# Optimization experiments

Measured on AMD Instinct MI355X. Metric: run time of the kernel, lower is better.

## Reference

```python
import jax, jax.numpy as jnp
import numpy as np

N_HEAD, D_MODEL, D_HEAD = 16, 1024, 64
LN_EPS = 1e-5
SCALE = 1.0 / (D_HEAD ** 0.5)


def _rel_shift(x):
    # x: [qlen, klen, bsz, n_head]
    q, k, b, n = x.shape
    zero_pad = jnp.zeros((q, 1, b, n), x.dtype)
    x_padded = jnp.concatenate([zero_pad, x], axis=1)        # [q, k+1, b, n]
    x_padded = x_padded.reshape(k + 1, q, b, n)
    return x_padded[1:].reshape(q, k, b, n)


def setup_inputs() -> dict:
    key = jax.random.key(0)
    ks = jax.random.split(key, 8)
    qlen, bsz = 2048, 4
    H = N_HEAD * D_HEAD
    s = 0.02
    return {
        "w": jax.random.normal(ks[0], (qlen, bsz, D_MODEL), jnp.float32),
        "r": jax.random.normal(ks[1], (qlen, D_MODEL), jnp.float32),
        "qkv_w": jax.random.normal(ks[2], (3 * H, D_MODEL), jnp.float32) * s,
        "r_net_w": jax.random.normal(ks[3], (H, D_MODEL), jnp.float32) * s,
        "o_w": jax.random.normal(ks[4], (D_MODEL, H), jnp.float32) * s,
        "r_w_bias": jax.random.normal(ks[5], (N_HEAD, D_HEAD), jnp.float32) * s,
        "r_r_bias": jax.random.normal(ks[6], (N_HEAD, D_HEAD), jnp.float32) * s,
        "ln_g": jnp.ones((D_MODEL,), jnp.float32),
        "ln_b": jnp.zeros((D_MODEL,), jnp.float32),
    }


def _layer_norm(x, g, b):
    mu = jnp.mean(x, axis=-1, keepdims=True)
    var = jnp.var(x, axis=-1, keepdims=True)
    return (x - mu) * jax.lax.rsqrt(var + LN_EPS) * g + b


def reference(w, r, qkv_w, r_net_w, o_w, r_w_bias, r_r_bias, ln_g, ln_b):
    qlen, bsz, _ = w.shape
    rlen = r.shape[0]
    H = N_HEAD * D_HEAD

    w_heads = jnp.einsum('ibm,hm->ibh', w, qkv_w)            # [q,b,3H]
    r_head_k = jnp.einsum('jm,hm->jh', r, r_net_w)           # [r,H]

    w_head_q = w_heads[..., :H].reshape(qlen, bsz, N_HEAD, D_HEAD)
    w_head_k = w_heads[..., H:2 * H].reshape(qlen, bsz, N_HEAD, D_HEAD)
    w_head_v = w_heads[..., 2 * H:].reshape(qlen, bsz, N_HEAD, D_HEAD)
    r_head_k = r_head_k.reshape(rlen, N_HEAD, D_HEAD)

    AC = jnp.einsum('ibnd,jbnd->ijbn', w_head_q + r_w_bias, w_head_k)
    BD = jnp.einsum('ibnd,jnd->ijbn', w_head_q + r_r_bias, r_head_k)
    BD = _rel_shift(BD)

    attn_score = (AC + BD) * SCALE                           # [q,k,b,n]
    attn_prob = jax.nn.softmax(attn_score, axis=1)

    attn_vec = jnp.einsum('ijbn,jbnd->ibnd', attn_prob, w_head_v)
    attn_vec = attn_vec.reshape(qlen, bsz, H)
    attn_out = jnp.einsum('ibh,mh->ibm', attn_vec, o_w)

    return _layer_norm(w + attn_out, ln_g, ln_b)
```

## Files before the change

kernel.cpp:

```cpp
#include <hip/hip_runtime.h>
#include <hip/hip_bf16.h>
#include <stdint.h>

using bf16 = __hip_bfloat16;
typedef __attribute__((ext_vector_type(8))) short bf16x8;
typedef __attribute__((ext_vector_type(4))) float f32x4;
typedef __attribute__((ext_vector_type(2))) int i32x2;

#define SCALE 0.125f

__device__ __forceinline__ float b2f(bf16 x) { return __bfloat162float(x); }
__device__ __forceinline__ bf16 f2b(float x) { return __float2bfloat16(x); }

__device__ __forceinline__ void gll16(const void* g, void* l) {
  __builtin_amdgcn_global_load_lds((const __attribute__((address_space(1))) void*)g,
                                   (__attribute__((address_space(3))) void*)l, 16, 0, 0);
}

__device__ __forceinline__ bf16x8 cat64(i32x2 a, i32x2 b) {
  int4 v; v.x = a.x; v.y = a.y; v.z = b.x; v.w = b.y;
  return *(bf16x8*)&v;
}

__global__ __launch_bounds__(256) void cvt_kernel(const float* __restrict__ in, bf16* __restrict__ out, int n4) {
  int i = blockIdx.x * 256 + threadIdx.x;
  if (i >= n4) return;
  float4 v = ((const float4*)in)[i];
  alignas(8) bf16 o[4];
  o[0] = f2b(v.x); o[1] = f2b(v.y); o[2] = f2b(v.z); o[3] = f2b(v.w);
  ((uint2*)out)[i] = *(const uint2*)o;
}

template<int STORE_BF16>
__global__ __launch_bounds__(256) void gemm_bt(const bf16* __restrict__ A, const bf16* __restrict__ B,
                                               void* __restrict__ C, int M, int N, int K) {
  __shared__ bf16 As[128][72];
  __shared__ bf16 Bs[128][72];
  const int tid = threadIdx.x;
  const int lane = tid & 63;
  const int w = tid >> 6, wr = w >> 1, wc = w & 1;
  const int m0 = blockIdx.y * 128, n0 = blockIdx.x * 128;
  const int lr = lane & 15, lg = lane >> 4;
  f32x4 acc[4][4] = {};
  for (int k0 = 0; k0 < K; k0 += 64) {
    __syncthreads();
#pragma unroll
    for (int i = 0; i < 4; ++i) {
      int c = tid + i * 256;
      int row = c >> 3, seg = c & 7;
      *(int4*)&As[row][seg * 8] = *(const int4*)&A[(size_t)(m0 + row) * K + k0 + seg * 8];
      *(int4*)&Bs[row][seg * 8] = *(const int4*)&B[(size_t)(n0 + row) * K + k0 + seg * 8];
    }
    __syncthreads();
#pragma unroll
    for (int kk = 0; kk < 2; ++kk) {
      bf16x8 af[4], bfv[4];
#pragma unroll
      for (int m = 0; m < 4; ++m) af[m] = *(const bf16x8*)&As[wr * 64 + m * 16 + lr][kk * 32 + lg * 8];
#pragma unroll
      for (int n = 0; n < 4; ++n) bfv[n] = *(const bf16x8*)&Bs[wc * 64 + n * 16 + lr][kk * 32 + lg * 8];
#pragma unroll
      for (int m = 0; m < 4; ++m)
#pragma unroll
        for (int n = 0; n < 4; ++n)
          acc[m][n] = __builtin_amdgcn_mfma_f32_16x16x32_bf16(af[m], bfv[n], acc[m][n], 0, 0, 0);
    }
  }
#pragma unroll
  for (int m = 0; m < 4; ++m)
#pragma unroll
    for (int n = 0; n < 4; ++n)
#pragma unroll
      for (int r = 0; r < 4; ++r) {
        int row = m0 + wr * 64 + m * 16 + lg * 4 + r;
        int col = n0 + wc * 64 + n * 16 + lr;
        if (STORE_BF16) ((bf16*)C)[(size_t)row * N + col] = f2b(acc[m][n][r]);
        else            ((float*)C)[(size_t)row * N + col] = acc[m][n][r];
      }
}

__global__ __launch_bounds__(256) void flash_kernel(const bf16* __restrict__ wh, const bf16* __restrict__ rk,
                                                    const float* __restrict__ rwb, const float* __restrict__ rrb,
                                                    bf16* __restrict__ av) {
  const int bn = blockIdx.y;
  const int b = bn >> 4, n = bn & 15;
  const int q0 = blockIdx.x * 64;
  const int tid = threadIdx.x, lane = tid & 63, w = tid >> 6;
  const int lr = lane & 15, lg = lane >> 4;
  __shared__ bf16 VtA[2 * 4096];
  __shared__ bf16 Ps[64][64];
  __shared__ bf16 Tp[64][128];

  bf16x8 qf[2], qrf[2][2];
#pragma unroll
  for (int kk = 0; kk < 2; ++kk) {
    {
      int row = q0 + w * 16 + lr;
      int4 raw = *(const int4*)&wh[((size_t)row * 4 + b) * 3072 + n * 64 + kk * 32 + lg * 8];
      const bf16* rp = (const bf16*)&raw;
      alignas(16) bf16 ov[8];
#pragma unroll
      for (int e = 0; e < 8; ++e) ov[e] = f2b((b2f(rp[e]) + rwb[n * 64 + kk * 32 + lg * 8 + e]) * SCALE);
      qf[kk] = *(const bf16x8*)ov;
    }
#pragma unroll
    for (int ao = 0; ao < 2; ++ao) {
      int row = q0 + ao + w * 16 + lr; if (row > 2047) row = 2047;
      int4 raw = *(const int4*)&wh[((size_t)row * 4 + b) * 3072 + n * 64 + kk * 32 + lg * 8];
      const bf16* rp = (const bf16*)&raw;
      alignas(16) bf16 ov[8];
#pragma unroll
      for (int e = 0; e < 8; ++e) ov[e] = f2b((b2f(rp[e]) + rrb[n * 64 + kk * 32 + lg * 8 + e]) * SCALE);
      qrf[ao][kk] = *(const bf16x8*)ov;
    }
  }

  auto coords = [&](int u, int& pbase, int& sub) {
    int tt = 64 * u - q0;
    if (tt <= -64) { pbase = tt + 2048; sub = 0; } else { pbase = tt; sub = 2; }
  };

  auto panel_direct = [&](int pbase, int sub) {
    const int aidx = sub ? 1 : 0;
#pragma unroll
    for (int nt = 0; nt < 4; ++nt) {
      int c = pbase + nt * 16 + lr - sub;
      c = c < 0 ? 0 : (c > 2047 ? 2047 : c);
      f32x4 pacc = {};
      bf16x8 b0 = *(const bf16x8*)&rk[(size_t)c * 1024 + n * 64 + lg * 8];
      bf16x8 b1 = *(const bf16x8*)&rk[(size_t)c * 1024 + n * 64 + 32 + lg * 8];
      pacc = __builtin_amdgcn_mfma_f32_16x16x32_bf16(qrf[aidx][0], b0, pacc, 0, 0, 0);
      pacc = __builtin_amdgcn_mfma_f32_16x16x32_bf16(qrf[aidx][1], b1, pacc, 0, 0, 0);
      int cm = (pbase + nt * 16 + lr) & 127;
#pragma unroll
      for (int r = 0; r < 4; ++r) Tp[w * 16 + lg * 4 + r][cm] = f2b(pacc[r]);
    }
  };

  auto stage_v = [&](int j0, int bufi) {
#pragma unroll
    for (int i = 0; i < 2; ++i) {
      int c = tid + i * 256;
      int jj = ((c >> 3) & 15) * 4 + ((c >> 1) & 3);
      int d0 = (c >> 7) * 16 + (c & 1) * 8;
      gll16(&wh[((size_t)(j0 + jj) * 4 + b) * 3072 + 2048 + n * 64 + d0],
            &VtA[bufi * 4096 + (w * 64 + i * 256) * 8]);
    }
  };

  panel_direct(1984 - q0, 0);
  { int pb, sb; coords(0, pb, sb); panel_direct(pb, sb); }
  stage_v(0, 0);

  const unsigned vtb = (unsigned)(uintptr_t)(__attribute__((address_space(3))) bf16*)VtA
                       + (unsigned)(lg * 256 + lr * 2);
  const bf16* kbase = wh + (size_t)b * 3072 + 1024 + n * 64;

  float lrow[4] = {0.f, 0.f, 0.f, 0.f};
  f32x4 oacc[4] = {};

  __syncthreads();

  int buf = 0;
  for (int u = 0; u < 32; ++u) {
    const int j0 = u * 64;
    if (u < 31) stage_v(j0 + 64, buf ^ 1);

    float bd[4][4];
#pragma unroll
    for (int f = 0; f < 4; ++f) {
      int jj = j0 + f * 16 + lr;
#pragma unroll
      for (int r = 0; r < 4; ++r) {
        int i = q0 + w * 16 + lg * 4 + r;
        int uu = jj - i;
        if (uu != 1) {
          int cm = (uu >= 2 ? uu : uu - 1) & 127;
          bd[f][r] = b2f(Tp[w * 16 + lg * 4 + r][cm]);
        } else bd[f][r] = 0.f;
      }
    }
    f32x4 s[4] = {};
#pragma unroll
    for (int kk = 0; kk < 2; ++kk)
#pragma unroll
      for (int f = 0; f < 4; ++f) {
        bf16x8 kf = *(const bf16x8*)&kbase[(size_t)(j0 + f * 16 + lr) * 12288 + kk * 32 + lg * 8];
        s[f] = __builtin_amdgcn_mfma_f32_16x16x32_bf16(qf[kk], kf, s[f], 0, 0, 0);
      }
#pragma unroll
    for (int f = 0; f < 4; ++f)
#pragma unroll
      for (int r = 0; r < 4; ++r) {
        float p = __expf(s[f][r] + bd[f][r]);
        s[f][r] = p;
        lrow[r] += p;
      }
#pragma unroll
    for (int f = 0; f < 4; ++f)
#pragma unroll
      for (int r = 0; r < 4; ++r) {
        int row = w * 16 + lg * 4 + r;
        Ps[row][(f * 16 + lr) ^ ((row & 7) << 3)] = f2b(s[f][r]);
      }
    {
      unsigned va = vtb + (unsigned)(buf << 13);
      i32x2 t0, t1, t2, t3, t4, t5, t6, t7;
      bf16x8 pf;
#define TRRD(d_, o_) asm volatile("ds_read_b64_tr_b16 %0, %1 offset:" o_ : "=v"(d_) : "v"(va))
      pf = *(const bf16x8*)&Ps[w * 16 + lr][((0 * 4 + lg) ^ (lr & 7)) * 8];
      TRRD(t0, "0");    TRRD(t1, "128");
      TRRD(t2, "2048"); TRRD(t3, "2176");
      TRRD(t4, "4096"); TRRD(t5, "4224");
      TRRD(t6, "6144"); TRRD(t7, "6272");
      asm volatile("s_waitcnt lgkmcnt(0)" ::: "memory");
      __builtin_amdgcn_sched_barrier(0);
      oacc[0] = __builtin_amdgcn_mfma_f32_16x16x32_bf16(pf, cat64(t0, t1), oacc[0], 0, 0, 0);
      oacc[1] = __builtin_amdgcn_mfma_f32_16x16x32_bf16(pf, cat64(t2, t3), oacc[1], 0, 0, 0);
      oacc[2] = __builtin_amdgcn_mfma_f32_16x16x32_bf16(pf, cat64(t4, t5), oacc[2], 0, 0, 0);
      oacc[3] = __builtin_amdgcn_mfma_f32_16x16x32_bf16(pf, cat64(t6, t7), oacc[3], 0, 0, 0);
      pf = *(const bf16x8*)&Ps[w * 16 + lr][((1 * 4 + lg) ^ (lr & 7)) * 8];
      TRRD(t0, "1024"); TRRD(t1, "1152");
      TRRD(t2, "3072"); TRRD(t3, "3200");
      TRRD(t4, "5120"); TRRD(t5, "5248");
      TRRD(t6, "7168"); TRRD(t7, "7296");
      asm volatile("s_waitcnt lgkmcnt(0)" ::: "memory");
      __builtin_amdgcn_sched_barrier(0);
      oacc[0] = __builtin_amdgcn_mfma_f32_16x16x32_bf16(pf, cat64(t0, t1), oacc[0], 0, 0, 0);
      oacc[1] = __builtin_amdgcn_mfma_f32_16x16x32_bf16(pf, cat64(t2, t3), oacc[1], 0, 0, 0);
      oacc[2] = __builtin_amdgcn_mfma_f32_16x16x32_bf16(pf, cat64(t4, t5), oacc[2], 0, 0, 0);
      oacc[3] = __builtin_amdgcn_mfma_f32_16x16x32_bf16(pf, cat64(t6, t7), oacc[3], 0, 0, 0);
#undef TRRD
    }
    if (u < 31) {
      int pb, sb; coords(u + 1, pb, sb);
      panel_direct(pb, sb);
    }
    __syncthreads();
    buf ^= 1;
  }
#pragma unroll
  for (int r = 0; r < 4; ++r)
#pragma unroll
    for (int msk = 1; msk <= 8; msk <<= 1) lrow[r] += __shfl_xor(lrow[r], msk);
#pragma unroll
  for (int df = 0; df < 4; ++df)
#pragma unroll
    for (int r = 0; r < 4; ++r) {
      int i = q0 + w * 16 + lg * 4 + r;
      av[((size_t)i * 4 + b) * 1024 + n * 64 + df * 16 + lr] = f2b(oacc[df][r] / lrow[r]);
    }
}

__global__ __launch_bounds__(256) void ln_kernel(const float* __restrict__ w, const float* __restrict__ ao,
                                                 const float* __restrict__ g, const float* __restrict__ bb,
                                                 float* __restrict__ out) {
  const int row = blockIdx.x;
  const int t = threadIdx.x;
  const float4 wv = ((const float4*)(w + (size_t)row * 1024))[t];
  const float4 av = ((const float4*)(ao + (size_t)row * 1024))[t];
  float x0 = wv.x + av.x, x1 = wv.y + av.y, x2 = wv.z + av.z, x3 = wv.w + av.w;
  float s1 = x0 + x1 + x2 + x3;
  float s2 = x0 * x0 + x1 * x1 + x2 * x2 + x3 * x3;
#pragma unroll
  for (int m = 1; m <= 32; m <<= 1) { s1 += __shfl_xor(s1, m); s2 += __shfl_xor(s2, m); }
  __shared__ float red[8];
  const int lane = t & 63, wv2 = t >> 6;
  if (lane == 0) { red[wv2] = s1; red[4 + wv2] = s2; }
  __syncthreads();
  s1 = red[0] + red[1] + red[2] + red[3];
  s2 = red[4] + red[5] + red[6] + red[7];
  const float mu = s1 * (1.f / 1024.f);
  const float var = s2 * (1.f / 1024.f) - mu * mu;
  const float rr = rsqrtf(var + 1e-5f);
  const float4 gv = ((const float4*)g)[t];
  const float4 bv = ((const float4*)bb)[t];
  float4 o;
  o.x = (x0 - mu) * rr * gv.x + bv.x;
  o.y = (x1 - mu) * rr * gv.y + bv.y;
  o.z = (x2 - mu) * rr * gv.z + bv.z;
  o.w = (x3 - mu) * rr * gv.w + bv.w;
  ((float4*)(out + (size_t)row * 1024))[t] = o;
}

extern "C" void kernel_launch(void* const* d_in, const int* in_sizes, int n_in,
                              void* d_out, int out_size, void* d_ws, size_t ws_size,
                              hipStream_t stream) {
  const float* w    = (const float*)d_in[0];
  const float* r    = (const float*)d_in[1];
  const float* qkvw = (const float*)d_in[2];
  const float* rnw  = (const float*)d_in[3];
  const float* ow   = (const float*)d_in[4];
  const float* rwb  = (const float*)d_in[5];
  const float* rrb  = (const float*)d_in[6];
  const float* lng  = (const float*)d_in[7];
  const float* lnb  = (const float*)d_in[8];
  float* out = (float*)d_out;

  char* ws = (char*)d_ws;
  size_t off = 0;
  auto alloc = [&](size_t bytes) -> char* {
    char* p = ws + off; off += (bytes + 255) & ~((size_t)255); return p;
  };
  bf16*  wb  = (bf16*)alloc((size_t)8192 * 1024 * 2);
  bf16*  qb  = (bf16*)alloc((size_t)3072 * 1024 * 2);
  bf16*  rb  = (bf16*)alloc((size_t)2048 * 1024 * 2);
  bf16*  rnb = (bf16*)alloc((size_t)1024 * 1024 * 2);
  bf16*  owb = (bf16*)alloc((size_t)1024 * 1024 * 2);
  bf16*  wh  = (bf16*)alloc((size_t)8192 * 3072 * 2);
  bf16*  rkb = (bf16*)alloc((size_t)2048 * 1024 * 2);
  bf16*  avb = (bf16*)alloc((size_t)8192 * 1024 * 2);
  float* ao  = (float*)alloc((size_t)8192 * 1024 * 4);

  auto cvt = [&](const float* in, bf16* o, size_t nelem) {
    int n4 = (int)(nelem / 4);
    cvt_kernel<<<dim3((n4 + 255) / 256), dim3(256), 0, stream>>>(in, o, n4);
  };
  cvt(w, wb, (size_t)8192 * 1024);
  cvt(qkvw, qb, (size_t)3072 * 1024);
  cvt(r, rb, (size_t)2048 * 1024);
  cvt(rnw, rnb, (size_t)1024 * 1024);
  cvt(ow, owb, (size_t)1024 * 1024);

  gemm_bt<1><<<dim3(3072 / 128, 8192 / 128), dim3(256), 0, stream>>>(wb, qb, wh, 8192, 3072, 1024);
  gemm_bt<1><<<dim3(1024 / 128, 2048 / 128), dim3(256), 0, stream>>>(rb, rnb, rkb, 2048, 1024, 1024);

  flash_kernel<<<dim3(32, 64), dim3(256), 0, stream>>>(wh, rkb, rwb, rrb, avb);

  gemm_bt<0><<<dim3(1024 / 128, 8192 / 128), dim3(256), 0, stream>>>(avb, owb, ao, 8192, 1024, 1024);
  ln_kernel<<<dim3(8192), dim3(256), 0, stream>>>(w, ao, lng, lnb, out);
}
```

Measured before the change: 726.8 us.

## Remap flash blocks per XCD, halve P staging buffer, add MFMA priority hints

The flash attention grid is flattened and remapped so that all 32 query tiles of a (batch, head) pair land on the same XCD. This is meant to improve L2 reuse of that head's K, V and R data. The P tile is now staged in LDS in two 32-column halves with a new XOR swizzle, each half written just before its MFMA, which cuts LDS use and may raise occupancy. s_setprio is wrapped around the MFMA groups to favour matrix-issuing waves, at the cost of extra LDS write/read rounds per iteration.

```diff
diff --git a/kernel.cpp b/kernel.cpp
--- a/kernel.cpp
+++ b/kernel.cpp
@@ -82,13 +82,16 @@
 __global__ __launch_bounds__(256) void flash_kernel(const bf16* __restrict__ wh, const bf16* __restrict__ rk,
                                                     const float* __restrict__ rwb, const float* __restrict__ rrb,
                                                     bf16* __restrict__ av) {
-  const int bn = blockIdx.y;
+  const int hid = blockIdx.x;
+  const int xcd = hid & 7;
+  const int idx = hid >> 3;
+  const int bn = xcd + 8 * (idx >> 5);
+  const int q0 = (idx & 31) * 64;
   const int b = bn >> 4, n = bn & 15;
-  const int q0 = blockIdx.x * 64;
   const int tid = threadIdx.x, lane = tid & 63, w = tid >> 6;
   const int lr = lane & 15, lg = lane >> 4;
   __shared__ bf16 VtA[2 * 4096];
-  __shared__ bf16 Ps[64][64];
+  __shared__ bf16 Ps[64][32];
   __shared__ bf16 Tp[64][128];
 
   bf16x8 qf[2], qrf[2][2];
@@ -129,8 +132,10 @@
       f32x4 pacc = {};
       bf16x8 b0 = *(const bf16x8*)&rk[(size_t)c * 1024 + n * 64 + lg * 8];
       bf16x8 b1 = *(const bf16x8*)&rk[(size_t)c * 1024 + n * 64 + 32 + lg * 8];
+      __builtin_amdgcn_s_setprio(1);
       pacc = __builtin_amdgcn_mfma_f32_16x16x32_bf16(qrf[aidx][0], b0, pacc, 0, 0, 0);
       pacc = __builtin_amdgcn_mfma_f32_16x16x32_bf16(qrf[aidx][1], b1, pacc, 0, 0, 0);
+      __builtin_amdgcn_s_setprio(0);
       int cm = (pbase + nt * 16 + lr) & 127;
 #pragma unroll
       for (int r = 0; r < 4; ++r) Tp[w * 16 + lg * 4 + r][cm] = f2b(pacc[r]);
@@ -186,7 +191,9 @@
 #pragma unroll
       for (int f = 0; f < 4; ++f) {
         bf16x8 kf = *(const bf16x8*)&kbase[(size_t)(j0 + f * 16 + lr) * 12288 + kk * 32 + lg * 8];
+        __builtin_amdgcn_s_setprio(1);
         s[f] = __builtin_amdgcn_mfma_f32_16x16x32_bf16(qf[kk], kf, s[f], 0, 0, 0);
+        __builtin_amdgcn_s_setprio(0);
       }
 #pragma unroll
     for (int f = 0; f < 4; ++f)
@@ -195,41 +202,52 @@
         float p = __expf(s[f][r] + bd[f][r]);
         s[f][r] = p;
         lrow[r] += p;
-      }
-#pragma unroll
-    for (int f = 0; f < 4; ++f)
-#pragma unroll
-      for (int r = 0; r < 4; ++r) {
-        int row = w * 16 + lg * 4 + r;
-        Ps[row][(f * 16 + lr) ^ ((row & 7) << 3)] = f2b(s[f][r]);
       }
     {
       unsigned va = vtb + (unsigned)(buf << 13);
       i32x2 t0, t1, t2, t3, t4, t5, t6, t7;
       bf16x8 pf;
 #define TRRD(d_, o_) asm volatile("ds_read_b64_tr_b16 %0, %1 offset:" o_ : "=v"(d_) : "v"(va))
-      pf = *(const bf16x8*)&Ps[w * 16 + lr][((0 * 4 + lg) ^ (lr & 7)) * 8];
+#pragma unroll
+      for (int f = 0; f < 2; ++f)
+#pragma unroll
+        for (int r = 0; r < 4; ++r) {
+          int row = w * 16 + lg * 4 + r;
+          Ps[row][(f * 16 + lr) ^ (lg << 3)] = f2b(s[f][r]);
+        }
+      pf = *(const bf16x8*)&Ps[w * 16 + lr][(lg ^ ((lr >> 2) & 3)) * 8];
       TRRD(t0, "0");    TRRD(t1, "128");
       TRRD(t2, "2048"); TRRD(t3, "2176");
       TRRD(t4, "4096"); TRRD(t5, "4224");
       TRRD(t6, "6144"); TRRD(t7, "6272");
       asm volatile("s_waitcnt lgkmcnt(0)" ::: "memory");
       __builtin_amdgcn_sched_barrier(0);
+      __builtin_amdgcn_s_setprio(1);
       oacc[0] = __builtin_amdgcn_mfma_f32_16x16x32_bf16(pf, cat64(t0, t1), oacc[0], 0, 0, 0);
       oacc[1] = __builtin_amdgcn_mfma_f32_16x16x32_bf16(pf, cat64(t2, t3), oacc[1], 0, 0, 0);
       oacc[2] = __builtin_amdgcn_mfma_f32_16x16x32_bf16(pf, cat64(t4, t5), oacc[2], 0, 0, 0);
       oacc[3] = __builtin_amdgcn_mfma_f32_16x16x32_bf16(pf, cat64(t6, t7), oacc[3], 0, 0, 0);
-      pf = *(const bf16x8*)&Ps[w * 16 + lr][((1 * 4 + lg) ^ (lr & 7)) * 8];
+      __builtin_amdgcn_s_setprio(0);
+#pragma unroll
+      for (int f = 2; f < 4; ++f)
+#pragma unroll
+        for (int r = 0; r < 4; ++r) {
+          int row = w * 16 + lg * 4 + r;
+          Ps[row][((f - 2) * 16 + lr) ^ (lg << 3)] = f2b(s[f][r]);
+        }
+      pf = *(const bf16x8*)&Ps[w * 16 + lr][(lg ^ ((lr >> 2) & 3)) * 8];
       TRRD(t0, "1024"); TRRD(t1, "1152");
       TRRD(t2, "3072"); TRRD(t3, "3200");
       TRRD(t4, "5120"); TRRD(t5, "5248");
       TRRD(t6, "7168"); TRRD(t7, "7296");
       asm volatile("s_waitcnt lgkmcnt(0)" ::: "memory");
       __builtin_amdgcn_sched_barrier(0);
+      __builtin_amdgcn_s_setprio(1);
       oacc[0] = __builtin_amdgcn_mfma_f32_16x16x32_bf16(pf, cat64(t0, t1), oacc[0], 0, 0, 0);
       oacc[1] = __builtin_amdgcn_mfma_f32_16x16x32_bf16(pf, cat64(t2, t3), oacc[1], 0, 0, 0);
       oacc[2] = __builtin_amdgcn_mfma_f32_16x16x32_bf16(pf, cat64(t4, t5), oacc[2], 0, 0, 0);
       oacc[3] = __builtin_amdgcn_mfma_f32_16x16x32_bf16(pf, cat64(t6, t7), oacc[3], 0, 0, 0);
+      __builtin_amdgcn_s_setprio(0);
 #undef TRRD
     }
     if (u < 31) {
@@ -325,7 +343,7 @@
   gemm_bt<1><<<dim3(3072 / 128, 8192 / 128), dim3(256), 0, stream>>>(wb, qb, wh, 8192, 3072, 1024);
   gemm_bt<1><<<dim3(1024 / 128, 2048 / 128), dim3(256), 0, stream>>>(rb, rnb, rkb, 2048, 1024, 1024);
 
-  flash_kernel<<<dim3(32, 64), dim3(256), 0, stream>>>(wh, rkb, rwb, rrb, avb);
+  flash_kernel<<<dim3(2048), dim3(256), 0, stream>>>(wh, rkb, rwb, rrb, avb);
 
   gemm_bt<0><<<dim3(1024 / 128, 8192 / 128), dim3(256), 0, stream>>>(avb, owb, ao, 8192, 1024, 1024);
   ln_kernel<<<dim3(8192), dim3(256), 0, stream>>>(w, ao, lng, lnb, out);
```

Measured after the change: 719.5 us. Within noise of the previous version (-1.0%).
